# Kernel optimization log

Measured on AMD Instinct MI355X. Metric: run time of the kernel, lower is better.

Reference implementation:

```python
import jax, jax.numpy as jnp
import numpy as np
from jax import lax

C = 256
B, H, W = 8, 48, 48
DN = ('NCHW', 'OIHW', 'NCHW')


def setup_inputs() -> dict:
    key = jax.random.key(0)
    ks = jax.random.split(key, 20)
    s = 0.05
    d = {
        'x': jax.random.normal(ks[0], (B, C, H, W), jnp.float32),
        # 1x1 convs of AnchoredSelfAttention, stored as [out, in] matrices
        'wq': jax.random.normal(ks[1], (C, C), jnp.float32) * s,
        'bq': jnp.zeros((C,), jnp.float32),
        'wk': jax.random.normal(ks[2], (C, C), jnp.float32) * s,
        'bk': jnp.zeros((C,), jnp.float32),
        'wv': jax.random.normal(ks[3], (C, C), jnp.float32) * s,
        'bv': jnp.zeros((C,), jnp.float32),
        'wa': jax.random.normal(ks[4], (C, C), jnp.float32) * s,
        'ba': jnp.zeros((C,), jnp.float32),
        # global branch (squeeze-excite style)
        'g1w': jax.random.normal(ks[5], (C // 8, C), jnp.float32) * s,
        'g1b': jnp.zeros((C // 8,), jnp.float32),
        'g2w': jax.random.normal(ks[6], (C, C // 8), jnp.float32) * s,
        'g2b': jnp.zeros((C,), jnp.float32),
        # spectral branch: (1,7) then (7,1) convs
        's1w': jax.random.normal(ks[7], (C, C, 1, 7), jnp.float32) * s,
        's1b': jnp.zeros((C,), jnp.float32),
        's2w': jax.random.normal(ks[8], (C, C, 7, 1), jnp.float32) * s,
        's2b': jnp.zeros((C,), jnp.float32),
        # local branch: 3x3 conv
        'lw': jax.random.normal(ks[9], (C, C, 3, 3), jnp.float32) * s,
        'lb': jnp.zeros((C,), jnp.float32),
    }
    return d


def _conv1x1(x, w, b):
    # x: [B,C,H,W], w: [O,C] -> [B,O,H,W]
    return jnp.einsum('bchw,oc->bohw', x, w) + b[None, :, None, None]


def _conv(x, w, b, pad):
    y = lax.conv_general_dilated(x, w, (1, 1), pad, dimension_numbers=DN)
    return y + b[None, :, None, None]


def reference(x, wq, bq, wk, bk, wv, bv, wa, ba,
              g1w, g1b, g2w, g2b, s1w, s1b, s2w, s2b, lw, lb):
    b, c, h, w = x.shape
    n = h * w

    # global branch: adaptive avg pool(1) + 2-layer bottleneck + sigmoid
    m = jnp.mean(x, axis=(2, 3))                       # [B,C]
    g = jax.nn.relu(m @ g1w.T + g1b)                   # [B,C/8]
    global_att = jax.nn.sigmoid(g @ g2w.T + g2b)[:, :, None, None]  # [B,C,1,1]

    # spectral branch: (1,7) conv + relu + (7,1) conv + sigmoid
    sb = jax.nn.relu(_conv(x, s1w, s1b, ((0, 0), (3, 3))))
    spectral_att = jax.nn.sigmoid(_conv(sb, s2w, s2b, ((3, 3), (0, 0))))

    # local branch: 3x3 conv + relu
    local_feat = jax.nn.relu(_conv(x, lw, lb, ((1, 1), (1, 1))))

    # anchored self-attention over full spatial grid (N = H*W)
    q = _conv1x1(x, wq, bq).reshape(b, c, n)           # [B,C,N]
    k = _conv1x1(x, wk, bk).reshape(b, c, n)
    v = _conv1x1(x, wv, bv).reshape(b, c, n)
    anchor = _conv1x1(x, wa, ba)
    scores = jnp.einsum('bcq,bck->bqk', q, k)          # [B,N,N]
    attn = jax.nn.softmax(scores, axis=-1)
    attended = jnp.einsum('bqk,bck->bcq', attn, v).reshape(b, c, h, w)
    attended_feat = x + attended + anchor

    return x * global_att + x * spectral_att + local_feat + attended_feat
```

## Files before the change

### kernel.cpp

```cpp
#include <hip/hip_runtime.h>


typedef unsigned short u16;
typedef unsigned int u32;
typedef __attribute__((ext_vector_type(8))) u16 u16x8;
typedef __attribute__((ext_vector_type(4))) float f32x4;
typedef __attribute__((ext_vector_type(4))) float f4;
typedef __attribute__((ext_vector_type(8))) __bf16 bf16x8;

#define DEVINL __device__ __forceinline__

constexpr int C = 256;
constexpr int N = 2304;
constexpr int HW = 48;
constexpr int BSTRIDE = C * N;
constexpr int BN = 8 * N;
constexpr int XPAD_ROWS = 54 * 54;
constexpr int SPAD_ROWS = 54 * 48;

DEVINL u16 f2bf(float f) {
  u32 u = __builtin_bit_cast(u32, f);
  u += 0x7fffu + ((u >> 16) & 1u);
  return (u16)(u >> 16);
}
DEVINL float bf2f(u16 h) {
  u32 u = ((u32)h) << 16;
  return __builtin_bit_cast(float, u);
}
DEVINL u16x8 ld8(const u16* p) { return *reinterpret_cast<const u16x8*>(p); }
DEVINL void st8(u16* p, u16x8 v) { *reinterpret_cast<u16x8*>(p) = v; }
DEVINL f32x4 mfma16(u16x8 a, u16x8 b, f32x4 c) {
  return __builtin_amdgcn_mfma_f32_16x16x32_bf16(
      __builtin_bit_cast(bf16x8, a), __builtin_bit_cast(bf16x8, b), c, 0, 0, 0);
}
DEVINL void gl16(const void* g, void* l) {
  __builtin_amdgcn_global_load_lds(
      (const __attribute__((address_space(1))) u32*)g,
      (__attribute__((address_space(3))) u32*)l, 16, 0, 0);
}

__global__ __launch_bounds__(256) void prep_kernel(
    const float* __restrict__ x,
    const float* __restrict__ wq, const float* __restrict__ wk,
    const float* __restrict__ wv, const float* __restrict__ wa,
    const float* __restrict__ s1w, const float* __restrict__ s2w,
    const float* __restrict__ lw,
    u16* __restrict__ xpad, u16* __restrict__ sbpad,
    u16* __restrict__ wqh, u16* __restrict__ wkh,
    u16* __restrict__ wvb, u16* __restrict__ wab,
    u16* __restrict__ s1rep, u16* __restrict__ s2rep, u16* __restrict__ lwrep,
    float* __restrict__ mb) {
  const int blk = blockIdx.x;
  const int t = threadIdx.x;
  if (blk < 704) {
    const long CX = (long)8 * XPAD_ROWS * C / 8;
    const long CS = (long)8 * SPAD_ROWS * C / 8;
    u16x8 z = {0, 0, 0, 0, 0, 0, 0, 0};
    for (long k = (long)blk * 256 + t; k < CX + CS; k += 704L * 256) {
      if (k < CX) st8(xpad + k * 8, z);
      else st8(sbpad + (k - CX) * 8, z);
    }
  } else if (blk < 960) {
    int base = (blk - 704) * 256 + t;
    wqh[base] = f2bf(wq[base]);
    wkh[base] = f2bf(wk[base]);
    wvb[base] = f2bf(wv[base]);
    wab[base] = f2bf(wa[base]);
    size_t b7 = (size_t)base * 7, b9 = (size_t)base * 9;
#pragma unroll
    for (int tp = 0; tp < 7; ++tp) s1rep[tp * 65536 + base] = f2bf(s1w[b7 + tp]);
#pragma unroll
    for (int tp = 0; tp < 7; ++tp) s2rep[tp * 65536 + base] = f2bf(s2w[b7 + tp]);
#pragma unroll
    for (int tp = 0; tp < 9; ++tp) lwrep[tp * 65536 + base] = f2bf(lw[b9 + tp]);
  } else {
    __shared__ float ws4[4];
    int r0 = (blk - 960) * 2;
#pragma unroll
    for (int rr = 0; rr < 2; ++rr) {
      const float* p = x + (size_t)(r0 + rr) * N;
      float s = 0.f;
      for (int i = t; i < N; i += 256) s += p[i];
#pragma unroll
      for (int off = 32; off >= 1; off >>= 1) s += __shfl_xor(s, off);
      if ((t & 63) == 0) ws4[t >> 6] = s;
      __syncthreads();
      if (t == 0) mb[r0 + rr] = (ws4[0] + ws4[1] + ws4[2] + ws4[3]) * (1.f / N);
      __syncthreads();
    }
  }
}

__global__ __launch_bounds__(256) void split_x_kernel(
    const float* __restrict__ x, u16* __restrict__ xhi,
    u16* __restrict__ xpad) {
  const int b = blockIdx.z;
  const int p0 = blockIdx.x * 64;
  const int c0 = blockIdx.y * 64;
  const int tid = threadIdx.x;
  __shared__ float tile[64][65];
#pragma unroll
  for (int it = 0; it < 4; ++it) {
    int idx = it * 256 + tid;
    int cr = idx >> 4, pc = (idx & 15) * 4;
    f4 v = *reinterpret_cast<const f4*>(&x[((size_t)b * C + c0 + cr) * N + p0 + pc]);
    tile[cr][pc] = v[0];
    tile[cr][pc + 1] = v[1];
    tile[cr][pc + 2] = v[2];
    tile[cr][pc + 3] = v[3];
  }
  __syncthreads();
#pragma unroll
  for (int it = 0; it < 2; ++it) {
    int idx = it * 256 + tid;
    int pr = idx >> 3, cg = (idx & 7) * 8;
    u16x8 h8;
#pragma unroll
    for (int j = 0; j < 8; ++j) h8[j] = f2bf(tile[cg + j][pr]);
    int p = p0 + pr;
    size_t o = ((size_t)b * N + p) * C + c0 + cg;
    st8(xhi + o, h8);
    int hh = p / HW, ww = p - hh * HW;
    size_t op = ((size_t)b * XPAD_ROWS + (size_t)(hh + 3) * 54 + ww + 3) * C + c0 + cg;
    st8(xpad + op, h8);
  }
}

__global__ __launch_bounds__(256) void global_kernel(
    const float* __restrict__ m, const float* __restrict__ g1w,
    const float* __restrict__ g1b, const float* __restrict__ g2w,
    const float* __restrict__ g2b, float* __restrict__ gatt) {
  int b = blockIdx.x, t = threadIdx.x;
  __shared__ float ms[256], hid[32];
  ms[t] = m[b * 256 + t];
  __syncthreads();
  if (t < 32) {
    float s = g1b[t];
    const float* wr = g1w + t * 256;
    for (int c2 = 0; c2 < 256; ++c2) s += ms[c2] * wr[c2];
    hid[t] = fmaxf(s, 0.f);
  }
  __syncthreads();
  float s = g2b[t];
#pragma unroll
  for (int j = 0; j < 32; ++j) s += hid[j] * g2w[t * 32 + j];
  gatt[b * 256 + t] = 1.f / (1.f + __expf(-s));
}

struct OpDesc {
  const u16* Xh;
  const u16* W;
  const float* bias;
  u16* o0;
  int tk;
  int act;
  int outn;
  int opad;
  int ips;
  int idy;
  int iox;
  int s0, s1;
};
struct OpPack {
  OpDesc d[6];
  int chunk;
  int ny;
};

__global__ __launch_bounds__(256, 2) void fused_gemm_kernel(OpPack pk) {
  const int swz = (blockIdx.x & 7) * pk.chunk + (blockIdx.x >> 3);
  const int xt = swz % 18;
  const int rest = swz / 18;
  const int y = rest % pk.ny;
  const int z = rest / pk.ny;
  const OpDesc dd = pk.d[y >> 1];
  const int mbase = xt * 128;
  const int nbase = (y & 1) * 128;
  const int tid = threadIdx.x;
  const int lane = tid & 63;
  const int wid = tid >> 6;
  const int wm = wid >> 1, wn = wid & 1;
  const int tk = dd.tk;
  const int NT = (tk == 0) ? 1 : ((tk == 3) ? 9 : 7);

  __shared__ __align__(16) u16 ldsX[2][128 * 64];
  __shared__ __align__(16) u16 ldsW[2][128 * 64];

  f32x4 acc[4][4];
#pragma unroll
  for (int m = 0; m < 4; ++m)
#pragma unroll
    for (int n = 0; n < 4; ++n) acc[m][n] = f32x4{0.f, 0.f, 0.f, 0.f};

  size_t xrow[4], wrow[4];
#pragma unroll
  for (int it = 0; it < 4; ++it) {
    int idx = it * 256 + tid;
    int rr = idx >> 3, ss = idx & 7;
    int perm = ss ^ (rr & 7);
    int p = mbase + rr;
    if (tk == 0) {
      xrow[it] = ((size_t)z * N + p) * 512 + (size_t)perm * 16;
    } else {
      int hh = p / HW, ww = p - hh * HW;
      xrow[it] = ((size_t)z * dd.ips + (size_t)(hh + 3) * dd.idy + ww + dd.iox) * 512 +
                 (size_t)perm * 16;
    }
    wrow[it] = ((size_t)(nbase + rr)) * 512 + (size_t)perm * 16;
  }
  int aoff[2][4], boff[2][4];
#pragma unroll
  for (int kk = 0; kk < 2; ++kk) {
    int seg = kk * 4 + (lane >> 4);
#pragma unroll
    for (int m = 0; m < 4; ++m) {
      int ra = wm * 64 + m * 16 + (lane & 15);
      aoff[kk][m] = ra * 64 + ((seg ^ (ra & 7)) << 3);
      int rb = wn * 64 + m * 16 + (lane & 15);
      boff[kk][m] = rb * 64 + ((seg ^ (rb & 7)) << 3);
    }
  }

  auto stage = [&](int buf, int tap, int ks) {
    const char* xs = (const char*)dd.Xh;
    const char* wsrc = (const char*)dd.W + (size_t)tap * 131072;
    int tsh = 0;
    if (tk == 1) tsh = tap - 3;
    else if (tk == 2) tsh = (tap - 3) * dd.idy;
    else if (tk == 3) tsh = (tap / 3 - 1) * dd.idy + (tap % 3 - 1);
    const long xadd = (long)tsh * 512 + ks * 128;
    const long wadd = ks * 128;
#pragma unroll
    for (int it = 0; it < 4; ++it) {
      gl16(xs + xrow[it] + xadd, &ldsX[buf][(it * 4 + wid) * 512]);
      gl16(wsrc + wrow[it] + wadd, &ldsW[buf][(it * 4 + wid) * 512]);
    }
  };

  int t0 = dd.s0;
  int cks = t0 & 3;
  int ctap = t0 >> 2;
  stage(0, ctap, cks);
  __syncthreads();
  int cur = 0;

#pragma unroll 1
  for (int t = dd.s0; t < dd.s1; ++t) {
    if (t + 1 < dd.s1) {
      if (++cks == 4) { cks = 0; ++ctap; }
      stage(cur ^ 1, ctap, cks);
    }
    const u16* Alds = dd.outn ? ldsW[cur] : ldsX[cur];
    const u16* Blds = dd.outn ? ldsX[cur] : ldsW[cur];
#pragma unroll
    for (int kk = 0; kk < 2; ++kk) {
      u16x8 af[4], bfr[4];
#pragma unroll
      for (int m = 0; m < 4; ++m) af[m] = ld8(&Alds[aoff[kk][m]]);
#pragma unroll
      for (int n = 0; n < 4; ++n) bfr[n] = ld8(&Blds[boff[kk][n]]);
      __builtin_amdgcn_s_setprio(1);
#pragma unroll
      for (int m = 0; m < 4; ++m)
#pragma unroll
        for (int n = 0; n < 4; ++n)
          acc[m][n] = mfma16(af[m], bfr[n], acc[m][n]);
      __builtin_amdgcn_s_setprio(0);
    }
    __syncthreads();
    cur ^= 1;
  }

  const int r4 = (lane >> 4) * 4, cl = lane & 15;
  const size_t xb = (size_t)z * BSTRIDE;
#pragma unroll
  for (int m = 0; m < 4; ++m) {
#pragma unroll
    for (int n = 0; n < 4; ++n) {
#pragma unroll
      for (int i = 0; i < 4; ++i) {
        int lrow = wm * 64 + m * 16 + r4 + i;
        int lcol = wn * 64 + n * 16 + cl;
        int o = dd.outn ? (nbase + lrow) : (nbase + lcol);
        int pos = dd.outn ? (mbase + lcol) : (mbase + lrow);
        float v = acc[m][n][i];
        if (dd.bias) {
          v += dd.bias[o];
          if (dd.act == 1) v = fmaxf(v, 0.f);
          else if (dd.act == 2) v = 1.f / (1.f + __expf(-v));
        }
        size_t oi;
        if (dd.opad) {
          int hh = pos / HW, ww = pos - hh * HW;
          oi = ((size_t)z * SPAD_ROWS + (size_t)(hh + 3) * 48 + ww) * C + o;
        } else {
          oi = xb + (dd.outn ? ((size_t)o * N + pos) : ((size_t)pos * C + o));
        }
        dd.o0[oi] = f2bf(v);
      }
    }
  }
}

__global__ __launch_bounds__(256, 2) void flash_kernel(
    const u16* __restrict__ Qhi, const u16* __restrict__ Khi,
    const u16* __restrict__ Vb, u16* __restrict__ P0, u16* __restrict__ P1,
    u16* __restrict__ P2, u16* __restrict__ P3, float* __restrict__ ML) {
  const int b = blockIdx.y;
  const int split = blockIdx.z;
  const int q0 = blockIdx.x * 64;
  const int tid = threadIdx.x;
  const int lane = tid & 63;
  const int wid = tid >> 6;
  const int qbase = q0 + wid * 16;
  const int bb = b * N;
  const u16* Vp = Vb + (size_t)b * BSTRIDE;

  __shared__ __align__(16) u16 lds_kh[32 * 256];
  __shared__ __align__(16) u16 lds_v[256 * 32];
  __shared__ __align__(16) u16 p_lds[4][16 * 40];

  u16x8 qfh[8];
  {
    size_t base = ((size_t)(bb + qbase + (lane & 15))) * C + (lane >> 4) * 8;
#pragma unroll
    for (int kc = 0; kc < 8; ++kc) qfh[kc] = ld8(Qhi + base + kc * 32);
  }

  f32x4 o_acc[16];
#pragma unroll
  for (int j = 0; j < 16; ++j) o_acc[j] = f32x4{0.f, 0.f, 0.f, 0.f};
  float m_r[4] = {-1e30f, -1e30f, -1e30f, -1e30f};
  float l_r[4] = {0.f, 0.f, 0.f, 0.f};

  u16x8 skh[4], sv[4];
  const int kt0 = split * 18;
  auto issue = [&](int kt) {
    const int k0 = kt * 32;
#pragma unroll
    for (int it = 0; it < 4; ++it) {
      int idx = it * 256 + tid;
      int r = idx >> 5, s = idx & 31;
      skh[it] = ld8(Khi + (size_t)(bb + k0 + r) * C + s * 8);
      int c2 = idx >> 2, s2 = idx & 3;
      sv[it] = ld8(Vp + (size_t)c2 * N + k0 + s2 * 8);
    }
  };
  issue(kt0);

#pragma unroll 1
  for (int t2 = 0; t2 < 18; ++t2) {
    __syncthreads();
#pragma unroll
    for (int it = 0; it < 4; ++it) {
      int idx = it * 256 + tid;
      int r = idx >> 5, s = idx & 31;
      st8(&lds_kh[r * 256 + ((s ^ (r & 7)) << 3)], skh[it]);
      int c2 = idx >> 2, s2 = idx & 3;
      st8(&lds_v[c2 * 32 + ((s2 ^ ((c2 >> 1) & 3)) << 3)], sv[it]);
    }
    __syncthreads();
    if (t2 < 17) issue(kt0 + t2 + 1);

    f32x4 sa0 = {0.f, 0.f, 0.f, 0.f}, sa1 = {0.f, 0.f, 0.f, 0.f};
    __builtin_amdgcn_s_setprio(1);
#pragma unroll
    for (int kc = 0; kc < 8; ++kc) {
      int seg = kc * 4 + (lane >> 4);
      int r0 = lane & 15, r1 = 16 + (lane & 15);
      u16x8 b0 = ld8(&lds_kh[r0 * 256 + ((seg ^ (r0 & 7)) << 3)]);
      u16x8 b1 = ld8(&lds_kh[r1 * 256 + ((seg ^ (r1 & 7)) << 3)]);
      sa0 = mfma16(qfh[kc], b0, sa0);
      sa1 = mfma16(qfh[kc], b1, sa1);
    }
    __builtin_amdgcn_s_setprio(0);

    float tm[4];
#pragma unroll
    for (int i = 0; i < 4; ++i) {
      float v = fmaxf(sa0[i], sa1[i]);
      v = fmaxf(v, __shfl_xor(v, 1));
      v = fmaxf(v, __shfl_xor(v, 2));
      v = fmaxf(v, __shfl_xor(v, 4));
      v = fmaxf(v, __shfl_xor(v, 8));
      tm[i] = v;
    }
    bool need = (tm[0] > m_r[0] + 8.f) | (tm[1] > m_r[1] + 8.f) |
                (tm[2] > m_r[2] + 8.f) | (tm[3] > m_r[3] + 8.f);
    if (__any(need)) {
      float sc[4];
#pragma unroll
      for (int i = 0; i < 4; ++i) {
        float mn = fmaxf(m_r[i], tm[i]);
        sc[i] = __expf(m_r[i] - mn);
        m_r[i] = mn;
        l_r[i] *= sc[i];
      }
#pragma unroll
      for (int j = 0; j < 16; ++j) {
#pragma unroll
        for (int i = 0; i < 4; ++i) o_acc[j][i] *= sc[i];
      }
    }
    u16* pl = p_lds[wid];
#pragma unroll
    for (int i = 0; i < 4; ++i) {
      float p0 = __expf(sa0[i] - m_r[i]);
      float p1 = __expf(sa1[i] - m_r[i]);
      float rs = p0 + p1;
      rs += __shfl_xor(rs, 1);
      rs += __shfl_xor(rs, 2);
      rs += __shfl_xor(rs, 4);
      rs += __shfl_xor(rs, 8);
      l_r[i] += rs;
      int row = (lane >> 4) * 4 + i;
      pl[row * 40 + (lane & 15)] = f2bf(p0);
      pl[row * 40 + 16 + (lane & 15)] = f2bf(p1);
    }
    u16x8 pa = ld8(&pl[(lane & 15) * 40 + (lane >> 4) * 8]);
    __builtin_amdgcn_s_setprio(1);
#pragma unroll
    for (int cf = 0; cf < 16; ++cf) {
      int col = cf * 16 + (lane & 15);
      u16x8 bv = ld8(&lds_v[col * 32 + (((lane >> 4) ^ ((col >> 1) & 3)) << 3)]);
      o_acc[cf] = mfma16(pa, bv, o_acc[cf]);
    }
    __builtin_amdgcn_s_setprio(0);
  }

  float rl[4];
#pragma unroll
  for (int i = 0; i < 4; ++i) rl[i] = 1.f / l_r[i];
  u16* Pout = (split == 0) ? P0 : (split == 1) ? P1 : (split == 2) ? P2 : P3;
#pragma unroll
  for (int cf = 0; cf < 16; ++cf) {
#pragma unroll
    for (int i = 0; i < 4; ++i) {
      int q = qbase + (lane >> 4) * 4 + i;
      int c2 = cf * 16 + (lane & 15);
      Pout[(size_t)(bb + q) * C + c2] = f2bf(o_acc[cf][i] * rl[i]);
    }
  }
  if ((lane & 15) == 0) {
#pragma unroll
    for (int i = 0; i < 4; ++i) {
      int q = qbase + (lane >> 4) * 4 + i;
      ML[split * BN + bb + q] = m_r[i];
      ML[(4 + split) * BN + bb + q] = l_r[i];
    }
  }
}

__global__ __launch_bounds__(256) void compose_kernel(
    const float* __restrict__ x, const float* __restrict__ gatt,
    const u16* __restrict__ sp0, const u16* __restrict__ sp1,
    const float* __restrict__ s2b, const u16* __restrict__ localT,
    const u16* __restrict__ anchT, const u16* __restrict__ P0,
    const u16* __restrict__ P1, const u16* __restrict__ P2,
    const u16* __restrict__ P3, const float* __restrict__ ML,
    float* __restrict__ out) {
  const int b = blockIdx.y;
  const int p0 = blockIdx.x * 32;
  const int t = threadIdx.x;
  const int bb = b * N;
  __shared__ __align__(16) u16 lsA[32 * 72], lsL[32 * 72], lsO[32 * 72];
  __shared__ float aw[4][32];
  if (t < 32) {
    int gq = bb + p0 + t;
    float m0 = ML[gq], m1 = ML[BN + gq], m2 = ML[2 * BN + gq],
          m3 = ML[3 * BN + gq];
    float M = fmaxf(fmaxf(m0, m1), fmaxf(m2, m3));
    float w0 = ML[4 * BN + gq] * __expf(m0 - M);
    float w1 = ML[5 * BN + gq] * __expf(m1 - M);
    float w2 = ML[6 * BN + gq] * __expf(m2 - M);
    float w3 = ML[7 * BN + gq] * __expf(m3 - M);
    float inv = 1.f / (w0 + w1 + w2 + w3);
    aw[0][t] = w0 * inv;
    aw[1][t] = w1 * inv;
    aw[2][t] = w2 * inv;
    aw[3][t] = w3 * inv;
  }
#pragma unroll 1
  for (int cc = 0; cc < 4; ++cc) {
    const int c0 = cc * 64;
    __syncthreads();
    {
      int r = t >> 3, s = t & 7;
      size_t g = (size_t)(bb + p0 + r) * C + c0 + s * 8;
      u16x8 q0 = ld8(sp0 + g), q1 = ld8(sp1 + g), sa8;
#pragma unroll
      for (int j = 0; j < 8; ++j) {
        float v = bf2f(q0[j]) + bf2f(q1[j]) + s2b[c0 + s * 8 + j];
        sa8[j] = f2bf(1.f / (1.f + __expf(-v)));
      }
      st8(&lsA[r * 72 + s * 8], sa8);
      st8(&lsL[r * 72 + s * 8], ld8(localT + g));
      u16x8 a0 = ld8(P0 + g), a1 = ld8(P1 + g), a2 = ld8(P2 + g),
            a3 = ld8(P3 + g), an = ld8(anchT + g);
      float w0 = aw[0][r], w1 = aw[1][r], w2 = aw[2][r], w3 = aw[3][r];
      u16x8 om;
#pragma unroll
      for (int j = 0; j < 8; ++j)
        om[j] = f2bf(w0 * bf2f(a0[j]) + w1 * bf2f(a1[j]) + w2 * bf2f(a2[j]) +
                     w3 * bf2f(a3[j]) + bf2f(an[j]));
      st8(&lsO[r * 72 + s * 8], om);
    }
    __syncthreads();
    int pl = t & 31, cg = t >> 5;
    int p = p0 + pl;
#pragma unroll
    for (int j = 0; j < 8; ++j) {
      int c2 = c0 + cg * 8 + j;
      size_t xi = ((size_t)b * C + c2) * N + p;
      float xv = x[xi];
      float sa = bf2f(lsA[pl * 72 + (c2 - c0)]);
      float lf = bf2f(lsL[pl * 72 + (c2 - c0)]);
      float om = bf2f(lsO[pl * 72 + (c2 - c0)]);
      float ga = gatt[b * 256 + c2];
      out[xi] = xv * (1.f + ga + sa) + lf + om;
    }
  }
}

extern "C" void kernel_launch(void* const* d_in, const int* in_sizes, int n_in,
                              void* d_out, int out_size, void* d_ws,
                              size_t ws_size, hipStream_t stream) {
  (void)in_sizes; (void)n_in; (void)out_size; (void)ws_size;
  const float* x   = (const float*)d_in[0];
  const float* wq  = (const float*)d_in[1];
  const float* bq  = (const float*)d_in[2];
  const float* wk  = (const float*)d_in[3];
  const float* bk  = (const float*)d_in[4];
  const float* wv  = (const float*)d_in[5];
  const float* bv  = (const float*)d_in[6];
  const float* wa  = (const float*)d_in[7];
  const float* ba  = (const float*)d_in[8];
  const float* g1w = (const float*)d_in[9];
  const float* g1b = (const float*)d_in[10];
  const float* g2w = (const float*)d_in[11];
  const float* g2b = (const float*)d_in[12];
  const float* s1w = (const float*)d_in[13];
  const float* s1b = (const float*)d_in[14];
  const float* s2w = (const float*)d_in[15];
  const float* s2b = (const float*)d_in[16];
  const float* lw  = (const float*)d_in[17];
  const float* lb  = (const float*)d_in[18];
  float* out = (float*)d_out;

  char* w = (char*)d_ws;
  const size_t SZB = (size_t)8 * N * C * sizeof(u16);
  const size_t SZXP = (size_t)8 * XPAD_ROWS * C * sizeof(u16);
  const size_t SZSP = (size_t)8 * SPAD_ROWS * C * sizeof(u16);
  u16* xhiT   = (u16*)(w + 0 * SZB);
  u16* sp0    = (u16*)(w + 1 * SZB);
  u16* sp1    = (u16*)(w + 2 * SZB);
  u16* qhiT   = (u16*)(w + 3 * SZB);
  u16* khiT   = (u16*)(w + 4 * SZB);
  u16* vbuf   = (u16*)(w + 5 * SZB);
  u16* localT = (u16*)(w + 6 * SZB);
  u16* OTb    = (u16*)(w + 7 * SZB);
  u16* Pf0    = (u16*)(w + 8 * SZB);
  u16* Pf1    = (u16*)(w + 9 * SZB);
  u16* xpad   = (u16*)(w + 10 * SZB);
  u16* sbpad  = (u16*)(w + 10 * SZB + SZXP);
  char* wp = w + 10 * SZB + SZXP + SZSP;
  u16* wqh   = (u16*)(wp + 0);
  u16* wkh   = (u16*)(wp + 131072);
  u16* wvb   = (u16*)(wp + 262144);
  u16* wab   = (u16*)(wp + 393216);
  u16* s1rep = (u16*)(wp + 524288);
  u16* s2rep = (u16*)(wp + 1441792);
  u16* lwrep = (u16*)(wp + 2359296);
  float* mb    = (float*)(wp + 3538944);
  float* gattb = (float*)(wp + 3547136);
  float* ML    = (float*)(wp + 3555328);

  prep_kernel<<<1984, 256, 0, stream>>>(x, wq, wk, wv, wa, s1w, s2w, lw,
                                        xpad, sbpad, wqh, wkh, wvb, wab,
                                        s1rep, s2rep, lwrep, mb);
  split_x_kernel<<<dim3(36, 4, 8), 256, 0, stream>>>(x, xhiT, xpad);
  global_kernel<<<8, 256, 0, stream>>>(mb, g1w, g1b, g2w, g2b, gattb);

  OpPack pk;
  pk.d[0] = {xpad, lwrep, lb, localT, 3, 1, 0, 0, XPAD_ROWS, 54, 3, 0, 36};
  pk.d[1] = {xpad, s1rep, s1b, sbpad,  1, 1, 0, 1, XPAD_ROWS, 54, 3, 0, 28};
  pk.d[2] = {xhiT, wqh,   bq, qhiT,    0, 0, 0, 0, N, 0, 0, 0, 4};
  pk.d[3] = {xhiT, wkh,   bk, khiT,    0, 0, 0, 0, N, 0, 0, 0, 4};
  pk.d[4] = {xhiT, wvb,   bv, vbuf,    0, 0, 1, 0, N, 0, 0, 0, 4};
  pk.d[5] = {xhiT, wab,   ba, OTb,     0, 0, 0, 0, N, 0, 0, 0, 4};
  pk.chunk = 1728 / 8;
  pk.ny = 12;
  fused_gemm_kernel<<<dim3(1728), 256, 0, stream>>>(pk);

  OpPack pk2;
  pk2.d[0] = {sbpad, s2rep, nullptr, sp0, 2, 0, 0, 0, SPAD_ROWS, 48, 0, 0, 14};
  pk2.d[1] = {sbpad, s2rep, nullptr, sp1, 2, 0, 0, 0, SPAD_ROWS, 48, 0, 14, 28};
  pk2.chunk = 576 / 8;
  pk2.ny = 4;
  fused_gemm_kernel<<<dim3(576), 256, 0, stream>>>(pk2);

  flash_kernel<<<dim3(36, 8, 4), 256, 0, stream>>>(
      qhiT, khiT, vbuf, Pf0, Pf1, xpad, sbpad, ML);

  compose_kernel<<<dim3(72, 8), 256, 0, stream>>>(
      x, gattb, sp0, sp1, s2b, localT, OTb, Pf0, Pf1, xpad, sbpad, ML, out);
}
```

Baseline: 310.7 us.

## Single-buffer GEMM LDS for higher occupancy and compute softmax row sums via MFMA

The fused GEMM kernel drops its LDS double buffer, halving shared memory per block, and raises the launch bound to 3 blocks per CU. Loads for the next k-step now start only after compute finishes, with a barrier on each side. This trades the explicit load/compute overlap for more resident waves to hide latency. Separately, the attention kernel replaces the shuffle-based row-sum reduction of P with an MFMA against a vector of bf16 ones, which also makes the sum use the bf16-rounded probabilities.

```diff
diff --git a/kernel.cpp b/kernel.cpp
--- a/kernel.cpp
+++ b/kernel.cpp
@@ -167,7 +167,7 @@
   int ny;
 };
 
-__global__ __launch_bounds__(256, 2) void fused_gemm_kernel(OpPack pk) {
+__global__ __launch_bounds__(256, 3) void fused_gemm_kernel(OpPack pk) {
   const int swz = (blockIdx.x & 7) * pk.chunk + (blockIdx.x >> 3);
   const int xt = swz % 18;
   const int rest = swz / 18;
@@ -181,10 +181,9 @@
   const int wid = tid >> 6;
   const int wm = wid >> 1, wn = wid & 1;
   const int tk = dd.tk;
-  const int NT = (tk == 0) ? 1 : ((tk == 3) ? 9 : 7);
-
-  __shared__ __align__(16) u16 ldsX[2][128 * 64];
-  __shared__ __align__(16) u16 ldsW[2][128 * 64];
+
+  __shared__ __align__(16) u16 ldsX[128 * 64];
+  __shared__ __align__(16) u16 ldsW[128 * 64];
 
   f32x4 acc[4][4];
 #pragma unroll
@@ -221,7 +220,7 @@
     }
   }
 
-  auto stage = [&](int buf, int tap, int ks) {
+  auto stage = [&](int tap, int ks) {
     const char* xs = (const char*)dd.Xh;
     const char* wsrc = (const char*)dd.W + (size_t)tap * 131072;
     int tsh = 0;
@@ -232,26 +231,21 @@
     const long wadd = ks * 128;
 #pragma unroll
     for (int it = 0; it < 4; ++it) {
-      gl16(xs + xrow[it] + xadd, &ldsX[buf][(it * 4 + wid) * 512]);
-      gl16(wsrc + wrow[it] + wadd, &ldsW[buf][(it * 4 + wid) * 512]);
+      gl16(xs + xrow[it] + xadd, &ldsX[(it * 4 + wid) * 512]);
+      gl16(wsrc + wrow[it] + wadd, &ldsW[(it * 4 + wid) * 512]);
     }
   };
 
   int t0 = dd.s0;
   int cks = t0 & 3;
   int ctap = t0 >> 2;
-  stage(0, ctap, cks);
-  __syncthreads();
-  int cur = 0;
+  stage(ctap, cks);
 
 #pragma unroll 1
   for (int t = dd.s0; t < dd.s1; ++t) {
-    if (t + 1 < dd.s1) {
-      if (++cks == 4) { cks = 0; ++ctap; }
-      stage(cur ^ 1, ctap, cks);
-    }
-    const u16* Alds = dd.outn ? ldsW[cur] : ldsX[cur];
-    const u16* Blds = dd.outn ? ldsX[cur] : ldsW[cur];
+    __syncthreads();
+    const u16* Alds = dd.outn ? ldsW : ldsX;
+    const u16* Blds = dd.outn ? ldsX : ldsW;
 #pragma unroll
     for (int kk = 0; kk < 2; ++kk) {
       u16x8 af[4], bfr[4];
@@ -268,7 +262,10 @@
       __builtin_amdgcn_s_setprio(0);
     }
     __syncthreads();
-    cur ^= 1;
+    if (t + 1 < dd.s1) {
+      if (++cks == 4) { cks = 0; ++ctap; }
+      stage(ctap, cks);
+    }
   }
 
   const int r4 = (lane >> 4) * 4, cl = lane & 15;
@@ -326,12 +323,14 @@
 #pragma unroll
     for (int kc = 0; kc < 8; ++kc) qfh[kc] = ld8(Qhi + base + kc * 32);
   }
+  const u16x8 ones = {0x3F80, 0x3F80, 0x3F80, 0x3F80,
+                      0x3F80, 0x3F80, 0x3F80, 0x3F80};
 
   f32x4 o_acc[16];
 #pragma unroll
   for (int j = 0; j < 16; ++j) o_acc[j] = f32x4{0.f, 0.f, 0.f, 0.f};
   float m_r[4] = {-1e30f, -1e30f, -1e30f, -1e30f};
-  float l_r[4] = {0.f, 0.f, 0.f, 0.f};
+  f32x4 l_acc = {0.f, 0.f, 0.f, 0.f};
 
   u16x8 skh[4], sv[4];
   const int kt0 = split * 18;
@@ -394,7 +393,7 @@
         float mn = fmaxf(m_r[i], tm[i]);
         sc[i] = __expf(m_r[i] - mn);
         m_r[i] = mn;
-        l_r[i] *= sc[i];
+        l_acc[i] *= sc[i];
       }
 #pragma unroll
       for (int j = 0; j < 16; ++j) {
@@ -407,18 +406,13 @@
     for (int i = 0; i < 4; ++i) {
       float p0 = __expf(sa0[i] - m_r[i]);
       float p1 = __expf(sa1[i] - m_r[i]);
-      float rs = p0 + p1;
-      rs += __shfl_xor(rs, 1);
-      rs += __shfl_xor(rs, 2);
-      rs += __shfl_xor(rs, 4);
-      rs += __shfl_xor(rs, 8);
-      l_r[i] += rs;
       int row = (lane >> 4) * 4 + i;
       pl[row * 40 + (lane & 15)] = f2bf(p0);
       pl[row * 40 + 16 + (lane & 15)] = f2bf(p1);
     }
     u16x8 pa = ld8(&pl[(lane & 15) * 40 + (lane >> 4) * 8]);
     __builtin_amdgcn_s_setprio(1);
+    l_acc = mfma16(pa, ones, l_acc);
 #pragma unroll
     for (int cf = 0; cf < 16; ++cf) {
       int col = cf * 16 + (lane & 15);
@@ -430,7 +424,7 @@
 
   float rl[4];
 #pragma unroll
-  for (int i = 0; i < 4; ++i) rl[i] = 1.f / l_r[i];
+  for (int i = 0; i < 4; ++i) rl[i] = 1.f / l_acc[i];
   u16* Pout = (split == 0) ? P0 : (split == 1) ? P1 : (split == 2) ? P2 : P3;
 #pragma unroll
   for (int cf = 0; cf < 16; ++cf) {
@@ -446,7 +440,7 @@
     for (int i = 0; i < 4; ++i) {
       int q = qbase + (lane >> 4) * 4 + i;
       ML[split * BN + bb + q] = m_r[i];
-      ML[(4 + split) * BN + bb + q] = l_r[i];
+      ML[(4 + split) * BN + bb + q] = l_acc[i];
     }
   }
 }
```

Measured after the change: 251.6 us (median of 2 runs). -19.0%, faster.
